# Kernel optimization log

Measured on AMD Instinct MI355X. Metric: run time of the kernel, lower is better.

The kernel has to match this reference:

```python
import jax, jax.numpy as jnp
import numpy as np

FEATURES = 1024
NUM_HEADS = 16
HEAD_SIZE = FEATURES // NUM_HEADS
B, T = 4, 2048
LN_EPS = 1e-6


def setup_inputs() -> dict:
    key = jax.random.key(0)
    ks = jax.random.split(key, 12)
    C, H, D = FEATURES, NUM_HEADS, HEAD_SIZE
    s_in = 1.0 / np.sqrt(C)
    s_ff = 1.0 / np.sqrt(4 * C)
    return {
        "x": jax.random.normal(ks[0], (B, T, C), jnp.float32),
        # per-head Q/K/V projections (no bias), stacked over heads
        "wq": jax.random.normal(ks[1], (H, C, D), jnp.float32) * s_in,
        "wk": jax.random.normal(ks[2], (H, C, D), jnp.float32) * s_in,
        "wv": jax.random.normal(ks[3], (H, C, D), jnp.float32) * s_in,
        "w_proj": jax.random.normal(ks[4], (C, C), jnp.float32) * s_in,
        "b_proj": jnp.zeros((C,), jnp.float32),
        "w_ff1": jax.random.normal(ks[5], (C, 4 * C), jnp.float32) * s_in,
        "b_ff1": jnp.zeros((4 * C,), jnp.float32),
        "w_ff2": jax.random.normal(ks[6], (4 * C, C), jnp.float32) * s_ff,
        "b_ff2": jnp.zeros((C,), jnp.float32),
        "ln1_scale": jnp.ones((C,), jnp.float32),
        "ln1_bias": jnp.zeros((C,), jnp.float32),
        "ln2_scale": jnp.ones((C,), jnp.float32),
        "ln2_bias": jnp.zeros((C,), jnp.float32),
    }


def _layernorm(x, scale, bias):
    mu = jnp.mean(x, axis=-1, keepdims=True)
    var = jnp.mean(jnp.square(x - mu), axis=-1, keepdims=True)
    return (x - mu) * jax.lax.rsqrt(var + LN_EPS) * scale + bias


def reference(x, wq, wk, wv, w_proj, b_proj, w_ff1, b_ff1, w_ff2, b_ff2,
              ln1_scale, ln1_bias, ln2_scale, ln2_bias):
    Bn, Tn, C = x.shape
    res = x
    xn = _layernorm(x, ln1_scale, ln1_bias)
    # per-head projections, vectorized over heads: [B,H,T,D]
    q = jnp.einsum('btc,hcd->bhtd', xn, wq)
    k = jnp.einsum('btc,hcd->bhtd', xn, wk)
    v = jnp.einsum('btc,hcd->bhtd', xn, wv)
    wei = jnp.einsum('bhtd,bhsd->bhts', q, k)
    tril = jnp.tril(jnp.ones((Tn, Tn), jnp.float32))
    # NOTE: original scales by C**-0.5 (full feature dim, not head_size),
    # and multiplies after masking (-inf * scale stays -inf).
    wei = jnp.where(tril == 0, -jnp.inf, wei) * (C ** -0.5)
    wei = jax.nn.softmax(wei, axis=-1)
    out = jnp.einsum('bhts,bhsd->bhtd', wei, v)
    # concat heads back to [B,T,C]
    out = out.transpose(0, 2, 1, 3).reshape(Bn, Tn, C)
    x = res + out @ w_proj + b_proj
    res = x
    xn = _layernorm(x, ln2_scale, ln2_bias)
    h = jax.nn.relu(xn @ w_ff1 + b_ff1)
    out = res + h @ w_ff2 + b_ff2
    return out
```

## Files before the change

### kernel.cpp

```cpp
#include <hip/hip_runtime.h>

#define Bn 4
#define Tn 2048
#define Cn 1024
#define Hn 16
#define Dn 64
#define Mr (Bn*Tn)

typedef _Float16 half8 __attribute__((ext_vector_type(8)));
typedef _Float16 half4v __attribute__((ext_vector_type(4)));
typedef float f32x4 __attribute__((ext_vector_type(4)));
typedef unsigned u32x4 __attribute__((ext_vector_type(4)));

__device__ __forceinline__ void g2l16(const void* g, void* l) {
  __builtin_amdgcn_global_load_lds((__attribute__((address_space(1))) void*)g,
                                   (__attribute__((address_space(3))) void*)l, 16, 0, 0);
}

__global__ __launch_bounds__(256) void transpose_f32_f16(const float* __restrict__ in,
                                                         _Float16* __restrict__ out,
                                                         int R, int C) {
  __shared__ float tile[32][33];
  const size_t zoff = (size_t)blockIdx.z * R * C;
  in += zoff; out += zoff;
  const int c0 = blockIdx.x * 32, r0 = blockIdx.y * 32;
  const int tx = threadIdx.x, ty = threadIdx.y;
#pragma unroll
  for (int i = 0; i < 4; ++i)
    tile[ty + i*8][tx] = in[(size_t)(r0 + ty + i*8) * C + c0 + tx];
  __syncthreads();
#pragma unroll
  for (int i = 0; i < 4; ++i)
    out[(size_t)(c0 + ty + i*8) * R + r0 + tx] = (_Float16)tile[tx][ty + i*8];
}

__global__ __launch_bounds__(256) void ln_row(const float* __restrict__ x,
                                              const float* __restrict__ g,
                                              const float* __restrict__ bta,
                                              _Float16* __restrict__ out) {
  const int row = blockIdx.x;
  const float4 v = ((const float4*)(x + (size_t)row * Cn))[threadIdx.x];
  float s  = v.x + v.y + v.z + v.w;
  float ss = v.x*v.x + v.y*v.y + v.z*v.z + v.w*v.w;
#pragma unroll
  for (int m = 1; m < 64; m <<= 1) { s += __shfl_xor(s, m); ss += __shfl_xor(ss, m); }
  __shared__ float red[8];
  const int wave = threadIdx.x >> 6, lane = threadIdx.x & 63;
  if (lane == 0) { red[wave] = s; red[4 + wave] = ss; }
  __syncthreads();
  s  = red[0] + red[1] + red[2] + red[3];
  ss = red[4] + red[5] + red[6] + red[7];
  const float mean = s * (1.0f/Cn);
  const float var  = ss * (1.0f/Cn) - mean*mean;
  const float rstd = rsqrtf(var + 1e-6f);
  const int c = threadIdx.x * 4;
  const float4 gg = ((const float4*)g)[threadIdx.x];
  const float4 bb = ((const float4*)bta)[threadIdx.x];
  half4v o;
  o[0] = (_Float16)((v.x - mean) * rstd * gg.x + bb.x);
  o[1] = (_Float16)((v.y - mean) * rstd * gg.y + bb.y);
  o[2] = (_Float16)((v.z - mean) * rstd * gg.z + bb.z);
  o[3] = (_Float16)((v.w - mean) * rstd * gg.w + bb.w);
  *((half4v*)(out + (size_t)row * Cn + c)) = o;
}

enum { EPI_QK = 0, EPI_V = 1, EPI_PROJ = 2, EPI_FF1 = 3, EPI_FF2 = 4 };

template<int EPI>
__global__ __launch_bounds__(256) void gemm_bt(const _Float16* __restrict__ A,
                                               const _Float16* __restrict__ Bt,
                                               void* __restrict__ outp,
                                               const float* __restrict__ bias,
                                               const float* __restrict__ resid,
                                               int M, int N, int K) {
  __shared__ __align__(16) _Float16 As[128*64];
  __shared__ __align__(16) _Float16 Bs[128*64];
  const int tid = threadIdx.x, wave = tid >> 6, lane = tid & 63;
  const int lr = lane & 15, lg = lane >> 4;
  const int brow = blockIdx.y * 128, bcol = blockIdx.x * 128;
  const int wrow = (wave >> 1) * 64, wcol = (wave & 1) * 64;
  f32x4 acc[4][4] = {};

  for (int kt = 0; kt < K; kt += 64) {
#pragma unroll
    for (int i = 0; i < 4; ++i) {
      const int chunk = i*4 + wave;
      const int e = chunk*512 + lane*8;
      const int rr = e >> 6, cc = e & 63;
      g2l16(A  + (size_t)(brow + rr)*K + kt + cc, As + chunk*512);
      g2l16(Bt + (size_t)(bcol + rr)*K + kt + cc, Bs + chunk*512);
    }
    __syncthreads();
#pragma unroll
    for (int kk = 0; kk < 64; kk += 32) {
      half8 af[4], bfr[4];
#pragma unroll
      for (int i = 0; i < 4; ++i) af[i]  = *(const half8*)(As + (wrow + i*16 + lr)*64 + kk + lg*8);
#pragma unroll
      for (int j = 0; j < 4; ++j) bfr[j] = *(const half8*)(Bs + (wcol + j*16 + lr)*64 + kk + lg*8);
#pragma unroll
      for (int i = 0; i < 4; ++i)
#pragma unroll
        for (int j = 0; j < 4; ++j)
          acc[i][j] = __builtin_amdgcn_mfma_f32_16x16x32_f16(af[i], bfr[j], acc[i][j], 0, 0, 0);
    }
    __syncthreads();
  }

  const int r0 = brow + wrow + lg*4;
  const int c0 = bcol + wcol + lr;
#pragma unroll
  for (int i = 0; i < 4; ++i) {
#pragma unroll
    for (int j = 0; j < 4; ++j) {
      const int col = c0 + j*16;
#pragma unroll
      for (int r = 0; r < 4; ++r) {
        const int row = r0 + i*16 + r;
        const float v = acc[i][j][r];
        if constexpr (EPI == EPI_QK) {
          ((_Float16*)outp)[(((size_t)(row >> 11) * Hn + (col >> 6)) * Tn + (row & 2047)) * Dn + (col & 63)] = (_Float16)v;
        } else if constexpr (EPI == EPI_V) {
          ((_Float16*)outp)[(((size_t)(row >> 11) * Hn + (col >> 6)) * Dn + (col & 63)) * Tn + (row & 2047)] = (_Float16)v;
        } else if constexpr (EPI == EPI_PROJ || EPI == EPI_FF2) {
          ((float*)outp)[(size_t)row * N + col] = v + bias[col] + resid[(size_t)row * N + col];
        } else if constexpr (EPI == EPI_FF1) {
          const float t = v + bias[col];
          ((_Float16*)outp)[(size_t)row * N + col] = (_Float16)(t > 0.f ? t : 0.f);
        }
      }
    }
  }
}

__global__ __launch_bounds__(256) void attn_kernel(const _Float16* __restrict__ q,
                                                   const _Float16* __restrict__ k,
                                                   const _Float16* __restrict__ vt,
                                                   _Float16* __restrict__ out) {
  const int pi = blockIdx.x;
  const int qtA = pi * 128;
  const int qtB = (15 - pi) * 128;
  const int h = blockIdx.y, b = blockIdx.z;
  const int tid = threadIdx.x, wave = tid >> 6, lane = tid & 63;
  const int lr = lane & 15, lg = lane >> 4;
  const size_t bh = (size_t)b * Hn + h;
  const _Float16* qg = q  + bh * (Tn * Dn);
  const _Float16* kg = k  + bh * (Tn * Dn);
  const _Float16* vg = vt + bh * (Dn * Tn);

  __shared__ __align__(16) _Float16 Ks[2][64*64];
  __shared__ __align__(16) _Float16 Vs[2][64*64];

  const _Float16 qsc = (_Float16)0.03125f;
  half8 qfA[2][2], qfB[2][2];
#pragma unroll
  for (int qi = 0; qi < 2; ++qi)
#pragma unroll
    for (int dh = 0; dh < 2; ++dh) {
      half8 a = *(const half8*)(qg + (size_t)(qtA + wave*32 + qi*16 + lr)*Dn + dh*32 + lg*8);
      half8 c = *(const half8*)(qg + (size_t)(qtB + wave*32 + qi*16 + lr)*Dn + dh*32 + lg*8);
#pragma unroll
      for (int j = 0; j < 8; ++j) { a[j] *= qsc; c[j] *= qsc; }
      qfA[qi][dh] = a; qfB[qi][dh] = c;
    }

  f32x4 oaccA[2][4] = {}, oaccB[2][4] = {};
  float mrowA[2] = {-__builtin_inff(), -__builtin_inff()};
  float mrowB[2] = {-__builtin_inff(), -__builtin_inff()};
  float lsumA[2] = {0.f, 0.f}, lsumB[2] = {0.f, 0.f};

  const int ntB = (qtB >> 6) + 2;

  auto STAGE = [&](int bufi, int t) {
    const int kvt = t * 64;
#pragma unroll
    for (int r = 0; r < 2; ++r) {
      const int g0 = r*256 + wave*64;
      const int g  = g0 + lane;
      const int rr = g >> 3;
      const int cs = (g & 7) ^ (rr & 7);
      g2l16(kg + (size_t)(kvt + rr)*Dn + cs*8, &Ks[bufi][g0*8]);
      g2l16(vg + (size_t)rr*Tn + kvt + cs*8,   &Vs[bufi][g0*8]);
    }
  };

  auto COMPUTE = [&](const half8 (&qf)[2][2], f32x4 (&oacc)[2][4],
                     float* mrow, float* lsum, int qb,
                     const _Float16* KS, const _Float16* VS, int kvt) {
    half8 kb[4][2];
#pragma unroll
    for (int f = 0; f < 4; ++f)
#pragma unroll
      for (int dh = 0; dh < 2; ++dh)
        kb[f][dh] = *(const half8*)(KS + (16*f + lr)*64 + (((4*dh + lg) ^ (lr & 7)) * 8));

#pragma unroll
    for (int qi = 0; qi < 2; ++qi) {
      f32x4 sv[4];
#pragma unroll
      for (int f = 0; f < 4; ++f) {
        f32x4 tacc = {0.f, 0.f, 0.f, 0.f};
        tacc = __builtin_amdgcn_mfma_f32_16x16x32_f16(kb[f][0], qf[qi][0], tacc, 0, 0, 0);
        tacc = __builtin_amdgcn_mfma_f32_16x16x32_f16(kb[f][1], qf[qi][1], tacc, 0, 0, 0);
        sv[f] = tacc;
      }
      const int qrow = qb + wave*32 + qi*16 + lr;
#pragma unroll
      for (int f = 0; f < 4; ++f)
#pragma unroll
        for (int r = 0; r < 4; ++r) {
          const int kvv = kvt + 16*f + 4*lg + r;
          sv[f][r] = (kvv > qrow) ? -__builtin_inff() : sv[f][r];
        }
      float tm = sv[0][0];
#pragma unroll
      for (int f = 0; f < 4; ++f)
#pragma unroll
        for (int r = 0; r < 4; ++r) tm = fmaxf(tm, sv[f][r]);
      tm = fmaxf(tm, __shfl_xor(tm, 16));
      tm = fmaxf(tm, __shfl_xor(tm, 32));
      const float mn = fmaxf(mrow[qi], tm);
      const float alpha = __expf(mrow[qi] - mn);
      mrow[qi] = mn;
      float ps = 0.f;
#pragma unroll
      for (int f = 0; f < 4; ++f)
#pragma unroll
        for (int r = 0; r < 4; ++r) {
          const float e = __expf(sv[f][r] - mn);
          ps += e;
          sv[f][r] = e;
        }
      ps += __shfl_xor(ps, 16);
      ps += __shfl_xor(ps, 32);
      lsum[qi] = lsum[qi] * alpha + ps;
      unsigned ph[4][2];
#pragma unroll
      for (int f = 0; f < 4; ++f)
#pragma unroll
        for (int m = 0; m < 2; ++m) {
          const unsigned lo = (unsigned)__builtin_bit_cast(unsigned short, (_Float16)sv[f][2*m]);
          const unsigned hi = (unsigned)__builtin_bit_cast(unsigned short, (_Float16)sv[f][2*m + 1]);
          ph[f][m] = lo | (hi << 16);
        }
      float ab[4];
#pragma unroll
      for (int r = 0; r < 4; ++r) ab[r] = __shfl(alpha, 4*lg + r);
#pragma unroll
      for (int df = 0; df < 4; ++df)
#pragma unroll
        for (int r = 0; r < 4; ++r) oacc[qi][df][r] *= ab[r];
      const int s0 = lr + 16*(2*(lg & 1));
      const int s1 = s0 + 16;
      half8 pa[2];
#pragma unroll
      for (int kh = 0; kh < 2; ++kh) {
        u32x4 w = {0u, 0u, 0u, 0u};
#pragma unroll
        for (int fi = 0; fi < 2; ++fi) {
          const unsigned a0 = __shfl(ph[2*kh + fi][0], s0);
          const unsigned a1 = __shfl(ph[2*kh + fi][1], s0);
          const unsigned a2 = __shfl(ph[2*kh + fi][0], s1);
          const unsigned a3 = __shfl(ph[2*kh + fi][1], s1);
          const bool sel = ((lg >> 1) == fi);
          w[0] = sel ? a0 : w[0];
          w[1] = sel ? a1 : w[1];
          w[2] = sel ? a2 : w[2];
          w[3] = sel ? a3 : w[3];
        }
        pa[kh] = __builtin_bit_cast(half8, w);
      }
#pragma unroll
      for (int df = 0; df < 4; ++df) {
        half8 vb0 = *(const half8*)(VS + (16*df + lr)*64 + (((0 + lg) ^ (lr & 7)) * 8));
        half8 vb1 = *(const half8*)(VS + (16*df + lr)*64 + (((4 + lg) ^ (lr & 7)) * 8));
        oacc[qi][df] = __builtin_amdgcn_mfma_f32_16x16x32_f16(pa[0], vb0, oacc[qi][df], 0, 0, 0);
        oacc[qi][df] = __builtin_amdgcn_mfma_f32_16x16x32_f16(pa[1], vb1, oacc[qi][df], 0, 0, 0);
      }
    }
  };

  STAGE(0, 0);
  __syncthreads();

  for (int t = 0; t < ntB; ++t) {
    const int kvt = t * 64;
    if (t + 1 < ntB) STAGE((t + 1) & 1, t + 1);
    const _Float16* KS = Ks[t & 1];
    const _Float16* VS = Vs[t & 1];
    if (kvt <= qtA + wave*32 + 31) COMPUTE(qfA, oaccA, mrowA, lsumA, qtA, KS, VS, kvt);
    if (kvt <= qtB + wave*32 + 31) COMPUTE(qfB, oaccB, mrowB, lsumB, qtB, KS, VS, kvt);
    __syncthreads();
  }

  auto EPI = [&](const f32x4 (&oacc)[2][4], const float* lsum, int qb) {
#pragma unroll
    for (int qi = 0; qi < 2; ++qi) {
      const float linv = 1.0f / lsum[qi];
      float lb[4];
#pragma unroll
      for (int r = 0; r < 4; ++r) lb[r] = __shfl(linv, 4*lg + r);
#pragma unroll
      for (int df = 0; df < 4; ++df)
#pragma unroll
        for (int r = 0; r < 4; ++r) {
          const int row = qb + wave*32 + qi*16 + 4*lg + r;
          const int col = h*Dn + df*16 + lr;
          out[((size_t)b*Tn + row)*Cn + col] = (_Float16)(oacc[qi][df][r] * lb[r]);
        }
    }
  };
  EPI(oaccA, lsumA, qtA);
  EPI(oaccB, lsumB, qtB);
}

extern "C" void kernel_launch(void* const* d_in, const int* in_sizes, int n_in,
                              void* d_out, int out_size, void* d_ws, size_t ws_size,
                              hipStream_t stream) {
  const float* x      = (const float*)d_in[0];
  const float* wq     = (const float*)d_in[1];
  const float* wk     = (const float*)d_in[2];
  const float* wv     = (const float*)d_in[3];
  const float* w_proj = (const float*)d_in[4];
  const float* b_proj = (const float*)d_in[5];
  const float* w_ff1  = (const float*)d_in[6];
  const float* b_ff1  = (const float*)d_in[7];
  const float* w_ff2  = (const float*)d_in[8];
  const float* b_ff2  = (const float*)d_in[9];
  const float* ln1s   = (const float*)d_in[10];
  const float* ln1b   = (const float*)d_in[11];
  const float* ln2s   = (const float*)d_in[12];
  const float* ln2b   = (const float*)d_in[13];
  float* outp = (float*)d_out;

  char* ws = (char*)d_ws;
  constexpr size_t MB = (size_t)1 << 20;
  _Float16* Wq_t  = (_Float16*)(ws + 0*MB);
  _Float16* Wk_t  = (_Float16*)(ws + 2*MB);
  _Float16* Wv_t  = (_Float16*)(ws + 4*MB);
  _Float16* Wp_t  = (_Float16*)(ws + 6*MB);
  _Float16* Wf1_t = (_Float16*)(ws + 8*MB);
  _Float16* Wf2_t = (_Float16*)(ws + 16*MB);
  _Float16* xn    = (_Float16*)(ws + 24*MB);
  _Float16* attn_o= (_Float16*)(ws + 24*MB);
  _Float16* qbuf  = (_Float16*)(ws + 40*MB);
  _Float16* kbuf  = (_Float16*)(ws + 56*MB);
  _Float16* vtbuf = (_Float16*)(ws + 72*MB);
  _Float16* hbuf  = (_Float16*)(ws + 40*MB);
  float*    x2    = (float*)   (ws + 104*MB);
  _Float16* xn2   = (_Float16*)(ws + 136*MB);

  dim3 tb(32, 8);
  transpose_f32_f16<<<dim3(2, 32, 16), tb, 0, stream>>>(wq, Wq_t, 1024, 64);
  transpose_f32_f16<<<dim3(2, 32, 16), tb, 0, stream>>>(wk, Wk_t, 1024, 64);
  transpose_f32_f16<<<dim3(2, 32, 16), tb, 0, stream>>>(wv, Wv_t, 1024, 64);
  transpose_f32_f16<<<dim3(32, 32, 1), tb, 0, stream>>>(w_proj, Wp_t, 1024, 1024);
  transpose_f32_f16<<<dim3(128, 32, 1), tb, 0, stream>>>(w_ff1, Wf1_t, 1024, 4096);
  transpose_f32_f16<<<dim3(32, 128, 1), tb, 0, stream>>>(w_ff2, Wf2_t, 4096, 1024);

  ln_row<<<Mr, 256, 0, stream>>>(x, ln1s, ln1b, xn);

  gemm_bt<EPI_QK><<<dim3(8, 64), 256, 0, stream>>>(xn, Wq_t, qbuf, nullptr, nullptr, Mr, Cn, Cn);
  gemm_bt<EPI_QK><<<dim3(8, 64), 256, 0, stream>>>(xn, Wk_t, kbuf, nullptr, nullptr, Mr, Cn, Cn);
  gemm_bt<EPI_V ><<<dim3(8, 64), 256, 0, stream>>>(xn, Wv_t, vtbuf, nullptr, nullptr, Mr, Cn, Cn);

  attn_kernel<<<dim3(8, Hn, Bn), 256, 0, stream>>>(qbuf, kbuf, vtbuf, attn_o);

  gemm_bt<EPI_PROJ><<<dim3(8, 64), 256, 0, stream>>>(attn_o, Wp_t, x2, b_proj, x, Mr, Cn, Cn);

  ln_row<<<Mr, 256, 0, stream>>>(x2, ln2s, ln2b, xn2);

  gemm_bt<EPI_FF1><<<dim3(32, 64), 256, 0, stream>>>(xn2, Wf1_t, hbuf, b_ff1, nullptr, Mr, 4*Cn, Cn);
  gemm_bt<EPI_FF2><<<dim3(8, 64), 256, 0, stream>>>(hbuf, Wf2_t, outp, b_ff2, x2, Mr, Cn, 4*Cn);
}
```

Baseline: 620.6 us.

## Replace GEMM with double-buffered swizzled 8-wave kernel and fuse QKV projections

Result: no change. 614.6 us (-1.0%).

```diff
diff --git a/kernel.cpp b/kernel.cpp
--- a/kernel.cpp
+++ b/kernel.cpp
@@ -64,64 +64,101 @@
   *((half4v*)(out + (size_t)row * Cn + c)) = o;
 }
 
-enum { EPI_QK = 0, EPI_V = 1, EPI_PROJ = 2, EPI_FF1 = 3, EPI_FF2 = 4 };
-
-template<int EPI>
-__global__ __launch_bounds__(256) void gemm_bt(const _Float16* __restrict__ A,
-                                               const _Float16* __restrict__ Bt,
-                                               void* __restrict__ outp,
-                                               const float* __restrict__ bias,
-                                               const float* __restrict__ resid,
-                                               int M, int N, int K) {
-  __shared__ __align__(16) _Float16 As[128*64];
-  __shared__ __align__(16) _Float16 Bs[128*64];
+enum { EPI_QKV = 0, EPI_PROJ = 2, EPI_FF1 = 3, EPI_FF2 = 4 };
+
+template<int BN, int EPI>
+__global__ __launch_bounds__(512, 1) void gemm8(const _Float16* __restrict__ A,
+                                                const _Float16* __restrict__ Bt,
+                                                void* __restrict__ outp,
+                                                void* __restrict__ out2,
+                                                void* __restrict__ out3,
+                                                const float* __restrict__ bias,
+                                                const float* __restrict__ resid,
+                                                int M, int N, int K) {
+  constexpr int MI  = (BN == 256) ? 8 : 4;
+  constexpr int VMC = 4 + BN/64;
+  __shared__ __align__(16) _Float16 As[2][256*64];
+  __shared__ __align__(16) _Float16 Bs[2][BN*64];
+
   const int tid = threadIdx.x, wave = tid >> 6, lane = tid & 63;
   const int lr = lane & 15, lg = lane >> 4;
-  const int brow = blockIdx.y * 128, bcol = blockIdx.x * 128;
-  const int wrow = (wave >> 1) * 64, wcol = (wave & 1) * 64;
-  f32x4 acc[4][4] = {};
-
-  for (int kt = 0; kt < K; kt += 64) {
+  const int brow = blockIdx.y * 256, bcol = blockIdx.x * BN;
+  const int WROW = (BN == 256) ? (wave >> 2) * 128 : (wave >> 1) * 64;
+  const int WCOL = ((BN == 256) ? (wave & 3) : (wave & 1)) * 64;
+
+  f32x4 acc[MI][4] = {};
+
+  auto STG = [&](int buf, int kt) {
+    const int kc = kt * 64;
 #pragma unroll
     for (int i = 0; i < 4; ++i) {
-      const int chunk = i*4 + wave;
-      const int e = chunk*512 + lane*8;
-      const int rr = e >> 6, cc = e & 63;
-      g2l16(A  + (size_t)(brow + rr)*K + kt + cc, As + chunk*512);
-      g2l16(Bt + (size_t)(bcol + rr)*K + kt + cc, Bs + chunk*512);
-    }
-    __syncthreads();
-#pragma unroll
-    for (int kk = 0; kk < 64; kk += 32) {
-      half8 af[4], bfr[4];
-#pragma unroll
-      for (int i = 0; i < 4; ++i) af[i]  = *(const half8*)(As + (wrow + i*16 + lr)*64 + kk + lg*8);
-#pragma unroll
-      for (int j = 0; j < 4; ++j) bfr[j] = *(const half8*)(Bs + (wcol + j*16 + lr)*64 + kk + lg*8);
-#pragma unroll
-      for (int i = 0; i < 4; ++i)
+      const int g0 = i*512 + wave*64;
+      const int g = g0 + lane;
+      const int rr = g >> 3, cs = (g & 7) ^ (rr & 7);
+      g2l16(A + (size_t)(brow + rr)*K + kc + cs*8, &As[buf][g0*8]);
+    }
+#pragma unroll
+    for (int i = 0; i < BN/64; ++i) {
+      const int g0 = i*512 + wave*64;
+      const int g = g0 + lane;
+      const int rr = g >> 3, cs = (g & 7) ^ (rr & 7);
+      g2l16(Bt + (size_t)(bcol + rr)*K + kc + cs*8, &Bs[buf][g0*8]);
+    }
+  };
+
+  const int nt = K >> 6;
+  STG(0, 0);
+  for (int kt = 0; kt < nt; ++kt) {
+    const int buf = kt & 1;
+    if (kt + 1 < nt) {
+      STG(buf ^ 1, kt + 1);
+      asm volatile("s_waitcnt vmcnt(%0)" :: "i"(VMC) : "memory");
+    } else {
+      asm volatile("s_waitcnt vmcnt(0)" ::: "memory");
+    }
+    __builtin_amdgcn_s_barrier();
+    __builtin_amdgcn_sched_barrier(0);
+    const _Float16* AS = As[buf];
+    const _Float16* BS = Bs[buf];
+#pragma unroll
+    for (int kh = 0; kh < 2; ++kh) {
+      half8 af[MI], bfr[4];
+#pragma unroll
+      for (int i = 0; i < MI; ++i)
+        af[i] = *(const half8*)(AS + (WROW + i*16 + lr)*64 + (((4*kh + lg) ^ (lr & 7)) * 8));
+#pragma unroll
+      for (int j = 0; j < 4; ++j)
+        bfr[j] = *(const half8*)(BS + (WCOL + j*16 + lr)*64 + (((4*kh + lg) ^ (lr & 7)) * 8));
+      __builtin_amdgcn_s_setprio(1);
+#pragma unroll
+      for (int i = 0; i < MI; ++i)
 #pragma unroll
         for (int j = 0; j < 4; ++j)
           acc[i][j] = __builtin_amdgcn_mfma_f32_16x16x32_f16(af[i], bfr[j], acc[i][j], 0, 0, 0);
-    }
-    __syncthreads();
+      __builtin_amdgcn_s_setprio(0);
+    }
+    __builtin_amdgcn_sched_barrier(0);
+    __builtin_amdgcn_s_barrier();
   }
 
-  const int r0 = brow + wrow + lg*4;
-  const int c0 = bcol + wcol + lr;
-#pragma unroll
-  for (int i = 0; i < 4; ++i) {
+#pragma unroll
+  for (int i = 0; i < MI; ++i) {
 #pragma unroll
     for (int j = 0; j < 4; ++j) {
-      const int col = c0 + j*16;
+      const int col = bcol + WCOL + j*16 + lr;
 #pragma unroll
       for (int r = 0; r < 4; ++r) {
-        const int row = r0 + i*16 + r;
+        const int row = brow + WROW + i*16 + lg*4 + r;
         const float v = acc[i][j][r];
-        if constexpr (EPI == EPI_QK) {
-          ((_Float16*)outp)[(((size_t)(row >> 11) * Hn + (col >> 6)) * Tn + (row & 2047)) * Dn + (col & 63)] = (_Float16)v;
-        } else if constexpr (EPI == EPI_V) {
-          ((_Float16*)outp)[(((size_t)(row >> 11) * Hn + (col >> 6)) * Dn + (col & 63)) * Tn + (row & 2047)] = (_Float16)v;
+        if constexpr (EPI == EPI_QKV) {
+          const int sel = col >> 10;
+          const int cw = col & 1023;
+          const int hh = cw >> 6, dd = cw & 63;
+          const size_t bhh = (size_t)(row >> 11) * Hn + hh;
+          const int t = row & 2047;
+          if (sel == 0)      ((_Float16*)outp)[(bhh*Tn + t)*Dn + dd] = (_Float16)v;
+          else if (sel == 1) ((_Float16*)out2)[(bhh*Tn + t)*Dn + dd] = (_Float16)v;
+          else               ((_Float16*)out3)[(bhh*Dn + dd)*Tn + t] = (_Float16)v;
         } else if constexpr (EPI == EPI_PROJ || EPI == EPI_FF2) {
           ((float*)outp)[(size_t)row * N + col] = v + bias[col] + resid[(size_t)row * N + col];
         } else if constexpr (EPI == EPI_FF1) {
@@ -360,16 +397,18 @@
 
   ln_row<<<Mr, 256, 0, stream>>>(x, ln1s, ln1b, xn);
 
-  gemm_bt<EPI_QK><<<dim3(8, 64), 256, 0, stream>>>(xn, Wq_t, qbuf, nullptr, nullptr, Mr, Cn, Cn);
-  gemm_bt<EPI_QK><<<dim3(8, 64), 256, 0, stream>>>(xn, Wk_t, kbuf, nullptr, nullptr, Mr, Cn, Cn);
-  gemm_bt<EPI_V ><<<dim3(8, 64), 256, 0, stream>>>(xn, Wv_t, vtbuf, nullptr, nullptr, Mr, Cn, Cn);
+  gemm8<128, EPI_QKV><<<dim3(24, 32), 512, 0, stream>>>(xn, Wq_t, qbuf, kbuf, vtbuf,
+                                                        nullptr, nullptr, Mr, 3*Cn, Cn);
 
   attn_kernel<<<dim3(8, Hn, Bn), 256, 0, stream>>>(qbuf, kbuf, vtbuf, attn_o);
 
-  gemm_bt<EPI_PROJ><<<dim3(8, 64), 256, 0, stream>>>(attn_o, Wp_t, x2, b_proj, x, Mr, Cn, Cn);
+  gemm8<128, EPI_PROJ><<<dim3(8, 32), 512, 0, stream>>>(attn_o, Wp_t, x2, nullptr, nullptr,
+                                                        b_proj, x, Mr, Cn, Cn);
 
   ln_row<<<Mr, 256, 0, stream>>>(x2, ln2s, ln2b, xn2);
 
-  gemm_bt<EPI_FF1><<<dim3(32, 64), 256, 0, stream>>>(xn2, Wf1_t, hbuf, b_ff1, nullptr, Mr, 4*Cn, Cn);
-  gemm_bt<EPI_FF2><<<dim3(8, 64), 256, 0, stream>>>(hbuf, Wf2_t, outp, b_ff2, x2, Mr, Cn, 4*Cn);
-}
+  gemm8<256, EPI_FF1><<<dim3(16, 32), 512, 0, stream>>>(xn2, Wf1_t, hbuf, nullptr, nullptr,
+                                                        b_ff1, nullptr, Mr, 4*Cn, Cn);
+  gemm8<128, EPI_FF2><<<dim3(8, 32), 512, 0, stream>>>(hbuf, Wf2_t, outp, nullptr, nullptr,
+                                                       b_ff2, x2, Mr, Cn, 4*Cn);
+}
```

## Replace GEMMs with 8-wave multi-stage pipelined kernel and fuse QKV projection

Applied to the files above, without the earlier changes.

Measured after the change: 592.7 us. 1.05x faster.

```diff
diff --git a/kernel.cpp b/kernel.cpp
--- a/kernel.cpp
+++ b/kernel.cpp
@@ -16,6 +16,14 @@
   __builtin_amdgcn_global_load_lds((__attribute__((address_space(1))) void*)g,
                                    (__attribute__((address_space(3))) void*)l, 16, 0, 0);
 }
+
+#define SB  __builtin_amdgcn_sched_barrier(0)
+#define BAR __builtin_amdgcn_s_barrier()
+#define VMW8 asm volatile("s_waitcnt vmcnt(8)" ::: "memory")
+#define VMW6 asm volatile("s_waitcnt vmcnt(6)" ::: "memory")
+#define VMW4 asm volatile("s_waitcnt vmcnt(4)" ::: "memory")
+#define VMW3 asm volatile("s_waitcnt vmcnt(3)" ::: "memory")
+#define VMW0 asm volatile("s_waitcnt vmcnt(0)" ::: "memory")
 
 __global__ __launch_bounds__(256) void transpose_f32_f16(const float* __restrict__ in,
                                                          _Float16* __restrict__ out,
@@ -64,64 +72,141 @@
   *((half4v*)(out + (size_t)row * Cn + c)) = o;
 }
 
-enum { EPI_QK = 0, EPI_V = 1, EPI_PROJ = 2, EPI_FF1 = 3, EPI_FF2 = 4 };
-
-template<int EPI>
-__global__ __launch_bounds__(256) void gemm_bt(const _Float16* __restrict__ A,
-                                               const _Float16* __restrict__ Bt,
-                                               void* __restrict__ outp,
-                                               const float* __restrict__ bias,
-                                               const float* __restrict__ resid,
-                                               int M, int N, int K) {
-  __shared__ __align__(16) _Float16 As[128*64];
-  __shared__ __align__(16) _Float16 Bs[128*64];
+enum { EPI_QKV = 0, EPI_PROJ = 2, EPI_FF1 = 3, EPI_FF2 = 4 };
+
+template<int BN, int EPI>
+__global__ __launch_bounds__(512, 2) void gemm8p(const _Float16* __restrict__ A,
+                                                 const _Float16* __restrict__ Bt,
+                                                 void* __restrict__ outp,
+                                                 void* __restrict__ out2,
+                                                 void* __restrict__ out3,
+                                                 const float* __restrict__ bias,
+                                                 const float* __restrict__ resid,
+                                                 int M, int N, int K, int nxg) {
+  constexpr int NF = BN/64;
+  constexpr int BSLOT = BN*32;
+  __shared__ __align__(16) _Float16 Ar[4*256*32];
+  __shared__ __align__(16) _Float16 Br[4*BSLOT];
+
   const int tid = threadIdx.x, wave = tid >> 6, lane = tid & 63;
   const int lr = lane & 15, lg = lane >> 4;
-  const int brow = blockIdx.y * 128, bcol = blockIdx.x * 128;
-  const int wrow = (wave >> 1) * 64, wcol = (wave & 1) * 64;
-  f32x4 acc[4][4] = {};
-
-  for (int kt = 0; kt < K; kt += 64) {
-#pragma unroll
-    for (int i = 0; i < 4; ++i) {
-      const int chunk = i*4 + wave;
-      const int e = chunk*512 + lane*8;
-      const int rr = e >> 6, cc = e & 63;
-      g2l16(A  + (size_t)(brow + rr)*K + kt + cc, As + chunk*512);
-      g2l16(Bt + (size_t)(bcol + rr)*K + kt + cc, Bs + chunk*512);
-    }
-    __syncthreads();
-#pragma unroll
-    for (int kk = 0; kk < 64; kk += 32) {
-      half8 af[4], bfr[4];
-#pragma unroll
-      for (int i = 0; i < 4; ++i) af[i]  = *(const half8*)(As + (wrow + i*16 + lr)*64 + kk + lg*8);
-#pragma unroll
-      for (int j = 0; j < 4; ++j) bfr[j] = *(const half8*)(Bs + (wcol + j*16 + lr)*64 + kk + lg*8);
-#pragma unroll
-      for (int i = 0; i < 4; ++i)
-#pragma unroll
-        for (int j = 0; j < 4; ++j)
-          acc[i][j] = __builtin_amdgcn_mfma_f32_16x16x32_f16(af[i], bfr[j], acc[i][j], 0, 0, 0);
-    }
-    __syncthreads();
+  const int sL = (lr & 3) ^ ((lr >> 2) & 3);
+  const int laneoff = lr*32 + ((lg ^ sL) * 8);
+
+  int lin = blockIdx.x;
+  const int cpx = gridDim.x >> 3;
+  lin = (lin & 7) * cpx + (lin >> 3);
+  const int bx = lin % nxg, by = lin / nxg;
+  const int brow = by * 256, bcol = bx * BN;
+  const int wr = wave >> 2, wc = wave & 3;
+  const int arow0 = wr * 128;
+  const int bcol0 = wc * (BN/4);
+
+  f32x4 acc[8][NF] = {};
+
+  auto STAGE = [&](int st, int kh) {
+    const int slot = (2*st + kh) & 3;
+    const int koff = st*64 + kh*32;
+#pragma unroll
+    for (int i = 0; i < 2; ++i) {
+      const int qc = i*512 + wave*64 + lane;
+      const int row = qc >> 2;
+      const int c = (qc & 3) ^ ((row & 3) ^ ((row >> 2) & 3));
+      g2l16(A + (size_t)(brow + row)*K + koff + c*8,
+            &Ar[slot*8192 + (i*512 + wave*64)*8]);
+    }
+#pragma unroll
+    for (int i = 0; i < BN/128; ++i) {
+      const int qc = i*512 + wave*64 + lane;
+      const int row = qc >> 2;
+      const int c = (qc & 3) ^ ((row & 3) ^ ((row >> 2) & 3));
+      g2l16(Bt + (size_t)(bcol + row)*K + koff + c*8,
+            &Br[slot*BSLOT + (i*512 + wave*64)*8]);
+    }
+  };
+  auto RDA = [&](int slot, int mh, half8* af) {
+#pragma unroll
+    for (int i = 0; i < 4; ++i)
+      af[i] = *(const half8*)(&Ar[slot*8192 + (arow0 + (mh*4 + i)*16)*32 + laneoff]);
+  };
+  auto RDB = [&](int slot, half8* bf) {
+#pragma unroll
+    for (int j = 0; j < NF; ++j)
+      bf[j] = *(const half8*)(&Br[slot*BSLOT + (bcol0 + j*16)*32 + laneoff]);
+  };
+
+#define MMC(MH) do {                                                          \
+    __builtin_amdgcn_s_setprio(1);                                            \
+    _Pragma("unroll") for (int i_ = 0; i_ < 4; ++i_)                          \
+      _Pragma("unroll") for (int j_ = 0; j_ < NF; ++j_)                       \
+        acc[(MH)*4 + i_][j_] = __builtin_amdgcn_mfma_f32_16x16x32_f16(        \
+            af[i_], bf[j_], acc[(MH)*4 + i_][j_], 0, 0, 0);                   \
+    __builtin_amdgcn_s_setprio(0); } while (0)
+
+  const int ns = K >> 6;
+  STAGE(0, 0); STAGE(0, 1); STAGE(1, 0);
+  if constexpr (BN == 256) VMW8; else VMW6;
+  SB; BAR;
+
+  half8 af[4], bf[NF];
+  for (int s = 0; s < ns - 2; ++s) {
+    const int s0 = (2*s) & 3, s1 = s0 + 1;
+    RDB(s0, bf); RDA(s0, 0, af); STAGE(s + 1, 1);
+    SB; BAR; MMC(0); SB; BAR;
+    RDA(s0, 1, af);
+    if constexpr (BN == 256) VMW8; else VMW6;
+    SB; BAR; MMC(1); SB; BAR;
+    RDB(s1, bf); RDA(s1, 0, af); STAGE(s + 2, 0);
+    SB; BAR; MMC(0); SB; BAR;
+    RDA(s1, 1, af);
+    if constexpr (BN == 256) VMW8; else VMW6;
+    SB; BAR; MMC(1); SB; BAR;
   }
-
-  const int r0 = brow + wrow + lg*4;
-  const int c0 = bcol + wcol + lr;
-#pragma unroll
-  for (int i = 0; i < 4; ++i) {
-#pragma unroll
-    for (int j = 0; j < 4; ++j) {
-      const int col = c0 + j*16;
+  {
+    const int s = ns - 2; const int s0 = (2*s) & 3, s1 = s0 + 1;
+    RDB(s0, bf); RDA(s0, 0, af); STAGE(s + 1, 1);
+    SB; BAR; MMC(0); SB; BAR;
+    RDA(s0, 1, af);
+    if constexpr (BN == 256) VMW8; else VMW6;
+    SB; BAR; MMC(1); SB; BAR;
+    RDB(s1, bf); RDA(s1, 0, af);
+    SB; BAR; MMC(0); SB; BAR;
+    RDA(s1, 1, af);
+    if constexpr (BN == 256) VMW4; else VMW3;
+    SB; BAR; MMC(1); SB; BAR;
+  }
+  {
+    const int s = ns - 1; const int s0 = (2*s) & 3, s1 = s0 + 1;
+    RDB(s0, bf); RDA(s0, 0, af);
+    SB; BAR; MMC(0); SB; BAR;
+    RDA(s0, 1, af);
+    VMW0;
+    SB; BAR; MMC(1); SB; BAR;
+    RDB(s1, bf); RDA(s1, 0, af);
+    SB; BAR; MMC(0); SB; BAR;
+    RDA(s1, 1, af);
+    SB; BAR; MMC(1); SB; BAR;
+  }
+#undef MMC
+
+#pragma unroll
+  for (int a = 0; a < 8; ++a) {
+#pragma unroll
+    for (int j = 0; j < NF; ++j) {
+      const int col = bcol + bcol0 + j*16 + lr;
 #pragma unroll
       for (int r = 0; r < 4; ++r) {
-        const int row = r0 + i*16 + r;
-        const float v = acc[i][j][r];
-        if constexpr (EPI == EPI_QK) {
-          ((_Float16*)outp)[(((size_t)(row >> 11) * Hn + (col >> 6)) * Tn + (row & 2047)) * Dn + (col & 63)] = (_Float16)v;
-        } else if constexpr (EPI == EPI_V) {
-          ((_Float16*)outp)[(((size_t)(row >> 11) * Hn + (col >> 6)) * Dn + (col & 63)) * Tn + (row & 2047)] = (_Float16)v;
+        const int row = brow + arow0 + a*16 + lg*4 + r;
+        const float v = acc[a][j][r];
+        if constexpr (EPI == EPI_QKV) {
+          const int sel = col >> 10;
+          const int cw = col & 1023;
+          const int hh = cw >> 6, dd = cw & 63;
+          const size_t bhh = (size_t)(row >> 11) * Hn + hh;
+          const int t = row & 2047;
+          if (sel == 0)      ((_Float16*)outp)[(bhh*Tn + t)*Dn + dd] = (_Float16)v;
+          else if (sel == 1) ((_Float16*)out2)[(bhh*Tn + t)*Dn + dd] = (_Float16)v;
+          else               ((_Float16*)out3)[(bhh*Dn + dd)*Tn + t] = (_Float16)v;
         } else if constexpr (EPI == EPI_PROJ || EPI == EPI_FF2) {
           ((float*)outp)[(size_t)row * N + col] = v + bias[col] + resid[(size_t)row * N + col];
         } else if constexpr (EPI == EPI_FF1) {
@@ -360,16 +445,18 @@
 
   ln_row<<<Mr, 256, 0, stream>>>(x, ln1s, ln1b, xn);
 
-  gemm_bt<EPI_QK><<<dim3(8, 64), 256, 0, stream>>>(xn, Wq_t, qbuf, nullptr, nullptr, Mr, Cn, Cn);
-  gemm_bt<EPI_QK><<<dim3(8, 64), 256, 0, stream>>>(xn, Wk_t, kbuf, nullptr, nullptr, Mr, Cn, Cn);
-  gemm_bt<EPI_V ><<<dim3(8, 64), 256, 0, stream>>>(xn, Wv_t, vtbuf, nullptr, nullptr, Mr, Cn, Cn);
+  gemm8p<256, EPI_QKV><<<dim3(384), 512, 0, stream>>>(xn, Wq_t, qbuf, kbuf, vtbuf,
+                                                      nullptr, nullptr, Mr, 3*Cn, Cn, 12);
 
   attn_kernel<<<dim3(8, Hn, Bn), 256, 0, stream>>>(qbuf, kbuf, vtbuf, attn_o);
 
-  gemm_bt<EPI_PROJ><<<dim3(8, 64), 256, 0, stream>>>(attn_o, Wp_t, x2, b_proj, x, Mr, Cn, Cn);
+  gemm8p<128, EPI_PROJ><<<dim3(256), 512, 0, stream>>>(attn_o, Wp_t, x2, nullptr, nullptr,
+                                                       b_proj, x, Mr, Cn, Cn, 8);
 
   ln_row<<<Mr, 256, 0, stream>>>(x2, ln2s, ln2b, xn2);
 
-  gemm_bt<EPI_FF1><<<dim3(32, 64), 256, 0, stream>>>(xn2, Wf1_t, hbuf, b_ff1, nullptr, Mr, 4*Cn, Cn);
-  gemm_bt<EPI_FF2><<<dim3(8, 64), 256, 0, stream>>>(hbuf, Wf2_t, outp, b_ff2, x2, Mr, Cn, 4*Cn);
-}
+  gemm8p<256, EPI_FF1><<<dim3(512), 512, 0, stream>>>(xn2, Wf1_t, hbuf, nullptr, nullptr,
+                                                      b_ff1, nullptr, Mr, 4*Cn, Cn, 16);
+  gemm8p<128, EPI_FF2><<<dim3(256), 512, 0, stream>>>(hbuf, Wf2_t, outp, nullptr, nullptr,
+                                                      b_ff2, x2, Mr, Cn, 4*Cn, 8);
+}
```
